# Performance work log

Hardware: AMD Instinct MI355X
Metric: run time of the kernel (lower is better)

## Reference

```python
import jax, jax.numpy as jnp
import numpy as np

NUM_FEATURE = 50


def setup_inputs() -> dict:
    key = jax.random.key(0)
    k1, = jax.random.split(key, 1)
    T = 500000
    query = jax.random.normal(k1, (T, NUM_FEATURE), dtype=jnp.float32)
    # Learned params exactly as the torch module initializes them:
    # ql.weight filled with 1 (shape [1, 50] -> we keep [50]), qW scalar 1.0
    ql_w = jnp.ones((NUM_FEATURE,), dtype=jnp.float32)
    qW = jnp.asarray(1.0, dtype=jnp.float32)
    return {"query": query, "ql_w": ql_w, "qW": qW}


def reference(query, ql_w, qW):
    # scores[i] = ql(tanh(qW * query[i]))  -> [T]
    scores = jnp.tanh(qW * query) @ ql_w
    # alpha = softmax(scores) over the T dimension (stable, single pass)
    alpha = jax.nn.softmax(scores, axis=0)
    # z = sum_i alpha[i] * query[i]  -> [NUM_FEATURE]
    z = alpha @ query
    return z
```

## Files before the change

kernel.cpp:

```cpp
#include <hip/hip_runtime.h>
#include <math.h>

#define NF 50
#define REC 52
#define NBLK 512
#define LOG2E 1.44269504f

#define DPP_QXOR1 0xB1
#define DPP_QXOR2 0x4E
#define DPP_ROR4  0x124
#define DPP_ROR8  0x128

__device__ __forceinline__ float dpp_add(float v, int ctrl) {
    float t;
    switch (ctrl) {
      case DPP_QXOR1: t = __int_as_float(__builtin_amdgcn_update_dpp(0, __float_as_int(v), DPP_QXOR1, 0xF, 0xF, true)); break;
      case DPP_QXOR2: t = __int_as_float(__builtin_amdgcn_update_dpp(0, __float_as_int(v), DPP_QXOR2, 0xF, 0xF, true)); break;
      case DPP_ROR4:  t = __int_as_float(__builtin_amdgcn_update_dpp(0, __float_as_int(v), DPP_ROR4,  0xF, 0xF, true)); break;
      default:        t = __int_as_float(__builtin_amdgcn_update_dpp(0, __float_as_int(v), DPP_ROR8,  0xF, 0xF, true)); break;
    }
    return v + t;
}

__global__ __launch_bounds__(512, 4) void attn_pass1(
    const float* __restrict__ query, const float* __restrict__ ql_w,
    const float* __restrict__ qWp, float* __restrict__ ws,
    int T, int totalGroups)
{
    const float qW = qWp[0];
    const int tid = threadIdx.x;
    const int q   = tid & 3;
    const int g   = blockIdx.x * 128 + (tid >> 2);

    float2 w01[7];
    #pragma unroll
    for (int t = 0; t < 6; ++t) {
        const int s = q + 4 * t;
        w01[t] = *(const float2*)(ql_w + 2 * s);
    }
    w01[6] = (q == 0) ? *(const float2*)(ql_w + 48) : make_float2(0.f, 0.f);
    const int d6 = (q == 0) ? 192 : 160;

    float sw = 0.f, saw = 0.f;
    #pragma unroll
    for (int t = 0; t < 7; ++t) {
        sw  += w01[t].x + w01[t].y;
        saw += fabsf(w01[t].x) + fabsf(w01[t].y);
    }
    sw  = dpp_add(dpp_add(sw,  DPP_QXOR1), DPP_QXOR2);
    saw = dpp_add(dpp_add(saw, DPP_QXOR1), DPP_QXOR2);
    const float M0  = (saw > 80.f) ? (saw - 80.f) : 0.f;
    const float c2  = 2.f * qW * LOG2E;
    const float K   = (sw - M0) * LOG2E;
    const float n2l = -2.f * LOG2E;

    float2 z[7];
    #pragma unroll
    for (int t = 0; t < 7; ++t) z[t] = make_float2(0.f, 0.f);
    float se = 0.f;

    const int G = totalGroups;
    const char* rp = (const char*)(query + (size_t)g * NF) + (q << 3);
    const size_t step = (size_t)G * NF * sizeof(float);

    for (int row = g; row < T; row += G, rp += step) {
        float2 x0 = *(const float2*)(rp);
        float2 x1 = *(const float2*)(rp + 32);
        float2 x2 = *(const float2*)(rp + 64);
        float2 x3 = *(const float2*)(rp + 96);
        float2 x4 = *(const float2*)(rp + 128);
        float2 x5 = *(const float2*)(rp + 160);
        float2 x6 = *(const float2*)(rp + d6);

        float p = 0.f;
        {
            float r;
            r = __builtin_amdgcn_rcpf(__builtin_amdgcn_exp2f(c2 * x0.x) + 1.f); p = fmaf(w01[0].x, r, p);
            r = __builtin_amdgcn_rcpf(__builtin_amdgcn_exp2f(c2 * x0.y) + 1.f); p = fmaf(w01[0].y, r, p);
            r = __builtin_amdgcn_rcpf(__builtin_amdgcn_exp2f(c2 * x1.x) + 1.f); p = fmaf(w01[1].x, r, p);
            r = __builtin_amdgcn_rcpf(__builtin_amdgcn_exp2f(c2 * x1.y) + 1.f); p = fmaf(w01[1].y, r, p);
            r = __builtin_amdgcn_rcpf(__builtin_amdgcn_exp2f(c2 * x2.x) + 1.f); p = fmaf(w01[2].x, r, p);
            r = __builtin_amdgcn_rcpf(__builtin_amdgcn_exp2f(c2 * x2.y) + 1.f); p = fmaf(w01[2].y, r, p);
            r = __builtin_amdgcn_rcpf(__builtin_amdgcn_exp2f(c2 * x3.x) + 1.f); p = fmaf(w01[3].x, r, p);
            r = __builtin_amdgcn_rcpf(__builtin_amdgcn_exp2f(c2 * x3.y) + 1.f); p = fmaf(w01[3].y, r, p);
            r = __builtin_amdgcn_rcpf(__builtin_amdgcn_exp2f(c2 * x4.x) + 1.f); p = fmaf(w01[4].x, r, p);
            r = __builtin_amdgcn_rcpf(__builtin_amdgcn_exp2f(c2 * x4.y) + 1.f); p = fmaf(w01[4].y, r, p);
            r = __builtin_amdgcn_rcpf(__builtin_amdgcn_exp2f(c2 * x5.x) + 1.f); p = fmaf(w01[5].x, r, p);
            r = __builtin_amdgcn_rcpf(__builtin_amdgcn_exp2f(c2 * x5.y) + 1.f); p = fmaf(w01[5].y, r, p);
            r = __builtin_amdgcn_rcpf(__builtin_amdgcn_exp2f(c2 * x6.x) + 1.f); p = fmaf(w01[6].x, r, p);
            r = __builtin_amdgcn_rcpf(__builtin_amdgcn_exp2f(c2 * x6.y) + 1.f); p = fmaf(w01[6].y, r, p);
        }
        p = dpp_add(dpp_add(p, DPP_QXOR1), DPP_QXOR2);
        const float e = __builtin_amdgcn_exp2f(fmaf(p, n2l, K));

        se += e;
        z[0].x = fmaf(e, x0.x, z[0].x); z[0].y = fmaf(e, x0.y, z[0].y);
        z[1].x = fmaf(e, x1.x, z[1].x); z[1].y = fmaf(e, x1.y, z[1].y);
        z[2].x = fmaf(e, x2.x, z[2].x); z[2].y = fmaf(e, x2.y, z[2].y);
        z[3].x = fmaf(e, x3.x, z[3].x); z[3].y = fmaf(e, x3.y, z[3].y);
        z[4].x = fmaf(e, x4.x, z[4].x); z[4].y = fmaf(e, x4.y, z[4].y);
        z[5].x = fmaf(e, x5.x, z[5].x); z[5].y = fmaf(e, x5.y, z[5].y);
        z[6].x = fmaf(e, x6.x, z[6].x); z[6].y = fmaf(e, x6.y, z[6].y);
    }

    #pragma unroll
    for (int t = 0; t < 7; ++t) {
        z[t].x = dpp_add(dpp_add(z[t].x, DPP_ROR4), DPP_ROR8);
        z[t].y = dpp_add(dpp_add(z[t].y, DPP_ROR4), DPP_ROR8);
    }
    se = dpp_add(dpp_add(se, DPP_ROR4), DPP_ROR8);

    __shared__ float sz[32][REC];
    if ((tid & 15) < 4) {
        const int eidx = tid >> 4;
        #pragma unroll
        for (int t = 0; t < 6; ++t) {
            const int s = q + 4 * t;
            *(float2*)&sz[eidx][2 * s] = z[t];
        }
        if (q == 0) {
            *(float2*)&sz[eidx][48] = z[6];
            sz[eidx][50] = se;
            sz[eidx][51] = 0.f;
        }
    }
    __syncthreads();

    if (tid < 51) {
        float acc = 0.f;
        #pragma unroll
        for (int h = 0; h < 32; ++h) acc += sz[h][tid];
        ws[(size_t)blockIdx.x * REC + tid] = acc;
    }
}

__global__ __launch_bounds__(1024) void attn_pass2(
    const float* __restrict__ ws, float* __restrict__ out, int B)
{
    __shared__ float zacc[16][REC];
    const int tid = threadIdx.x;
    const int w = tid >> 6, lane = tid & 63;

    if (lane < 51) {
        float acc = 0.f;
        int b = w;
        for (; b + 112 < B; b += 128) {
            acc += ws[(size_t)(b      ) * REC + lane]
                 + ws[(size_t)(b +  16) * REC + lane]
                 + ws[(size_t)(b +  32) * REC + lane]
                 + ws[(size_t)(b +  48) * REC + lane]
                 + ws[(size_t)(b +  64) * REC + lane]
                 + ws[(size_t)(b +  80) * REC + lane]
                 + ws[(size_t)(b +  96) * REC + lane]
                 + ws[(size_t)(b + 112) * REC + lane];
        }
        for (; b < B; b += 16)
            acc += ws[(size_t)b * REC + lane];
        zacc[w][lane] = acc;
    }
    __syncthreads();
    if (tid < NF) {
        float Z = 0.f, S = 0.f;
        #pragma unroll
        for (int h = 0; h < 16; ++h) { Z += zacc[h][tid]; S += zacc[h][50]; }
        out[tid] = Z / S;
    }
}

extern "C" void kernel_launch(void* const* d_in, const int* in_sizes, int n_in,
                              void* d_out, int out_size, void* d_ws, size_t ws_size,
                              hipStream_t stream) {
    const float* query = (const float*)d_in[0];
    const float* ql_w  = (const float*)d_in[1];
    const float* qW    = (const float*)d_in[2];
    float* out = (float*)d_out;
    float* ws  = (float*)d_ws;

    const int T = in_sizes[0] / NF;

    int B = NBLK;
    size_t need = (size_t)B * REC * sizeof(float);
    if (ws_size < need) {
        B = (int)(ws_size / (REC * sizeof(float)));
        if (B < 1) B = 1;
    }

    const int totalGroups = B * 128;
    hipLaunchKernelGGL(attn_pass1, dim3(B), dim3(512), 0, stream,
                       query, ql_w, qW, ws, T, totalGroups);
    hipLaunchKernelGGL(attn_pass2, dim3(1), dim3(1024), 0, stream,
                       ws, out, B);
}
```

Before: 25.71 us.

## Split each row across eight lanes instead of four and double block count

Result: slower. 27.88 us (+8.5%).

```diff
diff --git a/kernel.cpp b/kernel.cpp
--- a/kernel.cpp
+++ b/kernel.cpp
@@ -3,12 +3,12 @@
 
 #define NF 50
 #define REC 52
-#define NBLK 512
+#define NBLK 1024
 #define LOG2E 1.44269504f
 
 #define DPP_QXOR1 0xB1
 #define DPP_QXOR2 0x4E
-#define DPP_ROR4  0x124
+#define DPP_HMIRR 0x141
 #define DPP_ROR8  0x128
 
 __device__ __forceinline__ float dpp_add(float v, int ctrl) {
@@ -16,110 +16,86 @@
     switch (ctrl) {
       case DPP_QXOR1: t = __int_as_float(__builtin_amdgcn_update_dpp(0, __float_as_int(v), DPP_QXOR1, 0xF, 0xF, true)); break;
       case DPP_QXOR2: t = __int_as_float(__builtin_amdgcn_update_dpp(0, __float_as_int(v), DPP_QXOR2, 0xF, 0xF, true)); break;
-      case DPP_ROR4:  t = __int_as_float(__builtin_amdgcn_update_dpp(0, __float_as_int(v), DPP_ROR4,  0xF, 0xF, true)); break;
+      case DPP_HMIRR: t = __int_as_float(__builtin_amdgcn_update_dpp(0, __float_as_int(v), DPP_HMIRR, 0xF, 0xF, true)); break;
       default:        t = __int_as_float(__builtin_amdgcn_update_dpp(0, __float_as_int(v), DPP_ROR8,  0xF, 0xF, true)); break;
     }
     return v + t;
 }
 
-__global__ __launch_bounds__(512, 4) void attn_pass1(
+__global__ __launch_bounds__(512, 8) void attn_pass1(
     const float* __restrict__ query, const float* __restrict__ ql_w,
     const float* __restrict__ qWp, float* __restrict__ ws,
     int T, int totalGroups)
 {
     const float qW = qWp[0];
     const int tid = threadIdx.x;
-    const int q   = tid & 3;
-    const int g   = blockIdx.x * 128 + (tid >> 2);
+    const int l   = tid & 7;
+    const int g   = blockIdx.x * 64 + (tid >> 3);
 
-    float2 w01[7];
-    #pragma unroll
-    for (int t = 0; t < 6; ++t) {
-        const int s = q + 4 * t;
-        w01[t] = *(const float2*)(ql_w + 2 * s);
-    }
-    w01[6] = (q == 0) ? *(const float2*)(ql_w + 48) : make_float2(0.f, 0.f);
-    const int d6 = (q == 0) ? 192 : 160;
+    const float2 zf2 = make_float2(0.f, 0.f);
+    float2 w0 = *(const float2*)(ql_w + 2 * l);
+    float2 w1 = *(const float2*)(ql_w + 2 * (l + 8));
+    float2 w2 = *(const float2*)(ql_w + 2 * (l + 16));
+    float2 w3 = (l == 0) ? *(const float2*)(ql_w + 48) : zf2;
+    const int d3 = (l == 0) ? 192 : 128;
 
-    float sw = 0.f, saw = 0.f;
-    #pragma unroll
-    for (int t = 0; t < 7; ++t) {
-        sw  += w01[t].x + w01[t].y;
-        saw += fabsf(w01[t].x) + fabsf(w01[t].y);
-    }
-    sw  = dpp_add(dpp_add(sw,  DPP_QXOR1), DPP_QXOR2);
-    saw = dpp_add(dpp_add(saw, DPP_QXOR1), DPP_QXOR2);
+    float sw  = (w0.x + w0.y) + (w1.x + w1.y) + (w2.x + w2.y) + (w3.x + w3.y);
+    float saw = fabsf(w0.x) + fabsf(w0.y) + fabsf(w1.x) + fabsf(w1.y)
+              + fabsf(w2.x) + fabsf(w2.y) + fabsf(w3.x) + fabsf(w3.y);
+    sw  = dpp_add(dpp_add(dpp_add(sw,  DPP_QXOR1), DPP_QXOR2), DPP_HMIRR);
+    saw = dpp_add(dpp_add(dpp_add(saw, DPP_QXOR1), DPP_QXOR2), DPP_HMIRR);
     const float M0  = (saw > 80.f) ? (saw - 80.f) : 0.f;
     const float c2  = 2.f * qW * LOG2E;
     const float K   = (sw - M0) * LOG2E;
     const float n2l = -2.f * LOG2E;
 
-    float2 z[7];
-    #pragma unroll
-    for (int t = 0; t < 7; ++t) z[t] = make_float2(0.f, 0.f);
+    float2 z0 = zf2, z1 = zf2, z2 = zf2, z3 = zf2;
     float se = 0.f;
 
     const int G = totalGroups;
-    const char* rp = (const char*)(query + (size_t)g * NF) + (q << 3);
+    const char* rp = (const char*)(query + (size_t)g * NF) + (l << 3);
     const size_t step = (size_t)G * NF * sizeof(float);
 
     for (int row = g; row < T; row += G, rp += step) {
         float2 x0 = *(const float2*)(rp);
-        float2 x1 = *(const float2*)(rp + 32);
-        float2 x2 = *(const float2*)(rp + 64);
-        float2 x3 = *(const float2*)(rp + 96);
-        float2 x4 = *(const float2*)(rp + 128);
-        float2 x5 = *(const float2*)(rp + 160);
-        float2 x6 = *(const float2*)(rp + d6);
+        float2 x1 = *(const float2*)(rp + 64);
+        float2 x2 = *(const float2*)(rp + 128);
+        float2 x3 = *(const float2*)(rp + d3);
 
-        float p = 0.f;
-        {
-            float r;
-            r = __builtin_amdgcn_rcpf(__builtin_amdgcn_exp2f(c2 * x0.x) + 1.f); p = fmaf(w01[0].x, r, p);
-            r = __builtin_amdgcn_rcpf(__builtin_amdgcn_exp2f(c2 * x0.y) + 1.f); p = fmaf(w01[0].y, r, p);
-            r = __builtin_amdgcn_rcpf(__builtin_amdgcn_exp2f(c2 * x1.x) + 1.f); p = fmaf(w01[1].x, r, p);
-            r = __builtin_amdgcn_rcpf(__builtin_amdgcn_exp2f(c2 * x1.y) + 1.f); p = fmaf(w01[1].y, r, p);
-            r = __builtin_amdgcn_rcpf(__builtin_amdgcn_exp2f(c2 * x2.x) + 1.f); p = fmaf(w01[2].x, r, p);
-            r = __builtin_amdgcn_rcpf(__builtin_amdgcn_exp2f(c2 * x2.y) + 1.f); p = fmaf(w01[2].y, r, p);
-            r = __builtin_amdgcn_rcpf(__builtin_amdgcn_exp2f(c2 * x3.x) + 1.f); p = fmaf(w01[3].x, r, p);
-            r = __builtin_amdgcn_rcpf(__builtin_amdgcn_exp2f(c2 * x3.y) + 1.f); p = fmaf(w01[3].y, r, p);
-            r = __builtin_amdgcn_rcpf(__builtin_amdgcn_exp2f(c2 * x4.x) + 1.f); p = fmaf(w01[4].x, r, p);
-            r = __builtin_amdgcn_rcpf(__builtin_amdgcn_exp2f(c2 * x4.y) + 1.f); p = fmaf(w01[4].y, r, p);
-            r = __builtin_amdgcn_rcpf(__builtin_amdgcn_exp2f(c2 * x5.x) + 1.f); p = fmaf(w01[5].x, r, p);
-            r = __builtin_amdgcn_rcpf(__builtin_amdgcn_exp2f(c2 * x5.y) + 1.f); p = fmaf(w01[5].y, r, p);
-            r = __builtin_amdgcn_rcpf(__builtin_amdgcn_exp2f(c2 * x6.x) + 1.f); p = fmaf(w01[6].x, r, p);
-            r = __builtin_amdgcn_rcpf(__builtin_amdgcn_exp2f(c2 * x6.y) + 1.f); p = fmaf(w01[6].y, r, p);
-        }
-        p = dpp_add(dpp_add(p, DPP_QXOR1), DPP_QXOR2);
+        float p = 0.f, r;
+        r = __builtin_amdgcn_rcpf(__builtin_amdgcn_exp2f(c2 * x0.x) + 1.f); p = fmaf(w0.x, r, p);
+        r = __builtin_amdgcn_rcpf(__builtin_amdgcn_exp2f(c2 * x0.y) + 1.f); p = fmaf(w0.y, r, p);
+        r = __builtin_amdgcn_rcpf(__builtin_amdgcn_exp2f(c2 * x1.x) + 1.f); p = fmaf(w1.x, r, p);
+        r = __builtin_amdgcn_rcpf(__builtin_amdgcn_exp2f(c2 * x1.y) + 1.f); p = fmaf(w1.y, r, p);
+        r = __builtin_amdgcn_rcpf(__builtin_amdgcn_exp2f(c2 * x2.x) + 1.f); p = fmaf(w2.x, r, p);
+        r = __builtin_amdgcn_rcpf(__builtin_amdgcn_exp2f(c2 * x2.y) + 1.f); p = fmaf(w2.y, r, p);
+        r = __builtin_amdgcn_rcpf(__builtin_amdgcn_exp2f(c2 * x3.x) + 1.f); p = fmaf(w3.x, r, p);
+        r = __builtin_amdgcn_rcpf(__builtin_amdgcn_exp2f(c2 * x3.y) + 1.f); p = fmaf(w3.y, r, p);
+
+        p = dpp_add(dpp_add(dpp_add(p, DPP_QXOR1), DPP_QXOR2), DPP_HMIRR);
         const float e = __builtin_amdgcn_exp2f(fmaf(p, n2l, K));
 
         se += e;
-        z[0].x = fmaf(e, x0.x, z[0].x); z[0].y = fmaf(e, x0.y, z[0].y);
-        z[1].x = fmaf(e, x1.x, z[1].x); z[1].y = fmaf(e, x1.y, z[1].y);
-        z[2].x = fmaf(e, x2.x, z[2].x); z[2].y = fmaf(e, x2.y, z[2].y);
-        z[3].x = fmaf(e, x3.x, z[3].x); z[3].y = fmaf(e, x3.y, z[3].y);
-        z[4].x = fmaf(e, x4.x, z[4].x); z[4].y = fmaf(e, x4.y, z[4].y);
-        z[5].x = fmaf(e, x5.x, z[5].x); z[5].y = fmaf(e, x5.y, z[5].y);
-        z[6].x = fmaf(e, x6.x, z[6].x); z[6].y = fmaf(e, x6.y, z[6].y);
+        z0.x = fmaf(e, x0.x, z0.x); z0.y = fmaf(e, x0.y, z0.y);
+        z1.x = fmaf(e, x1.x, z1.x); z1.y = fmaf(e, x1.y, z1.y);
+        z2.x = fmaf(e, x2.x, z2.x); z2.y = fmaf(e, x2.y, z2.y);
+        z3.x = fmaf(e, x3.x, z3.x); z3.y = fmaf(e, x3.y, z3.y);
     }
 
-    #pragma unroll
-    for (int t = 0; t < 7; ++t) {
-        z[t].x = dpp_add(dpp_add(z[t].x, DPP_ROR4), DPP_ROR8);
-        z[t].y = dpp_add(dpp_add(z[t].y, DPP_ROR4), DPP_ROR8);
-    }
-    se = dpp_add(dpp_add(se, DPP_ROR4), DPP_ROR8);
+    z0.x = dpp_add(z0.x, DPP_ROR8); z0.y = dpp_add(z0.y, DPP_ROR8);
+    z1.x = dpp_add(z1.x, DPP_ROR8); z1.y = dpp_add(z1.y, DPP_ROR8);
+    z2.x = dpp_add(z2.x, DPP_ROR8); z2.y = dpp_add(z2.y, DPP_ROR8);
+    z3.x = dpp_add(z3.x, DPP_ROR8); z3.y = dpp_add(z3.y, DPP_ROR8);
+    se   = dpp_add(se,   DPP_ROR8);
 
     __shared__ float sz[32][REC];
-    if ((tid & 15) < 4) {
+    if ((tid & 15) < 8) {
         const int eidx = tid >> 4;
-        #pragma unroll
-        for (int t = 0; t < 6; ++t) {
-            const int s = q + 4 * t;
-            *(float2*)&sz[eidx][2 * s] = z[t];
-        }
-        if (q == 0) {
-            *(float2*)&sz[eidx][48] = z[6];
+        *(float2*)&sz[eidx][2 * l]        = z0;
+        *(float2*)&sz[eidx][2 * (l + 8)]  = z1;
+        *(float2*)&sz[eidx][2 * (l + 16)] = z2;
+        if (l == 0) {
+            *(float2*)&sz[eidx][48] = z3;
             sz[eidx][50] = se;
             sz[eidx][51] = 0.f;
         }
@@ -185,7 +161,7 @@
         if (B < 1) B = 1;
     }
 
-    const int totalGroups = B * 128;
+    const int totalGroups = B * 64;
     hipLaunchKernelGGL(attn_pass1, dim3(B), dim3(512), 0, stream,
                        query, ql_w, qW, ws, T, totalGroups);
     hipLaunchKernelGGL(attn_pass2, dim3(1), dim3(1024), 0, stream,
```

## Fuse two-pass reduction into one cooperative kernel with grid sync

Applied to the files above, without the earlier changes.

Result: slower. 92.12 us (+258.3%).

```diff
diff --git a/kernel.cpp b/kernel.cpp
--- a/kernel.cpp
+++ b/kernel.cpp
@@ -1,4 +1,5 @@
 #include <hip/hip_runtime.h>
+#include <hip/hip_cooperative_groups.h>
 #include <math.h>
 
 #define NF 50
@@ -22,10 +23,10 @@
     return v + t;
 }
 
-__global__ __launch_bounds__(512, 4) void attn_pass1(
+__global__ __launch_bounds__(512, 4) void attn_fused(
     const float* __restrict__ query, const float* __restrict__ ql_w,
     const float* __restrict__ qWp, float* __restrict__ ws,
-    int T, int totalGroups)
+    float* __restrict__ out, int T, int totalGroups, int nBlocks)
 {
     const float qW = qWp[0];
     const int tid = threadIdx.x;
@@ -132,38 +133,31 @@
         for (int h = 0; h < 32; ++h) acc += sz[h][tid];
         ws[(size_t)blockIdx.x * REC + tid] = acc;
     }
-}
 
-__global__ __launch_bounds__(1024) void attn_pass2(
-    const float* __restrict__ ws, float* __restrict__ out, int B)
-{
-    __shared__ float zacc[16][REC];
-    const int tid = threadIdx.x;
-    const int w = tid >> 6, lane = tid & 63;
+    cooperative_groups::this_grid().sync();
 
-    if (lane < 51) {
-        float acc = 0.f;
-        int b = w;
-        for (; b + 112 < B; b += 128) {
-            acc += ws[(size_t)(b      ) * REC + lane]
-                 + ws[(size_t)(b +  16) * REC + lane]
-                 + ws[(size_t)(b +  32) * REC + lane]
-                 + ws[(size_t)(b +  48) * REC + lane]
-                 + ws[(size_t)(b +  64) * REC + lane]
-                 + ws[(size_t)(b +  80) * REC + lane]
-                 + ws[(size_t)(b +  96) * REC + lane]
-                 + ws[(size_t)(b + 112) * REC + lane];
+    if (blockIdx.x == 0) {
+        const int w = tid >> 6, lane = tid & 63;
+        if (lane < 51) {
+            float acc = 0.f;
+            int b = w;
+            for (; b + 24 < nBlocks; b += 32) {
+                acc += ws[(size_t)(b     ) * REC + lane]
+                     + ws[(size_t)(b +  8) * REC + lane]
+                     + ws[(size_t)(b + 16) * REC + lane]
+                     + ws[(size_t)(b + 24) * REC + lane];
+            }
+            for (; b < nBlocks; b += 8)
+                acc += ws[(size_t)b * REC + lane];
+            sz[w][lane] = acc;
         }
-        for (; b < B; b += 16)
-            acc += ws[(size_t)b * REC + lane];
-        zacc[w][lane] = acc;
-    }
-    __syncthreads();
-    if (tid < NF) {
-        float Z = 0.f, S = 0.f;
-        #pragma unroll
-        for (int h = 0; h < 16; ++h) { Z += zacc[h][tid]; S += zacc[h][50]; }
-        out[tid] = Z / S;
+        __syncthreads();
+        if (tid < NF) {
+            float Z = 0.f, S = 0.f;
+            #pragma unroll
+            for (int h = 0; h < 8; ++h) { Z += sz[h][tid]; S += sz[h][50]; }
+            out[tid] = Z / S;
+        }
     }
 }
 
@@ -176,7 +170,7 @@
     float* out = (float*)d_out;
     float* ws  = (float*)d_ws;
 
-    const int T = in_sizes[0] / NF;
+    int T = in_sizes[0] / NF;
 
     int B = NBLK;
     size_t need = (size_t)B * REC * sizeof(float);
@@ -185,9 +179,9 @@
         if (B < 1) B = 1;
     }
 
-    const int totalGroups = B * 128;
-    hipLaunchKernelGGL(attn_pass1, dim3(B), dim3(512), 0, stream,
-                       query, ql_w, qW, ws, T, totalGroups);
-    hipLaunchKernelGGL(attn_pass2, dim3(1), dim3(1024), 0, stream,
-                       ws, out, B);
+    int totalGroups = B * 128;
+    void* args[] = { (void*)&query, (void*)&ql_w, (void*)&qW, (void*)&ws,
+                     (void*)&out, (void*)&T, (void*)&totalGroups, (void*)&B };
+    hipLaunchCooperativeKernel((void*)attn_fused, dim3(B), dim3(512),
+                               args, 0, stream);
 }
```

## Process row pairs with float4 loads in a new even-T pass1 kernel

Applied to the files above, without the earlier changes.

Result: slower. 26.51 us (+3.1%).

```diff
diff --git a/kernel.cpp b/kernel.cpp
--- a/kernel.cpp
+++ b/kernel.cpp
@@ -22,7 +22,9 @@
     return v + t;
 }
 
-__global__ __launch_bounds__(512, 4) void attn_pass1(
+#define RCPE(v) __builtin_amdgcn_rcpf(__builtin_amdgcn_exp2f(c2 * (v)) + 1.f)
+
+__global__ __launch_bounds__(512, 4) void attn_pass1_even(
     const float* __restrict__ query, const float* __restrict__ ql_w,
     const float* __restrict__ qWp, float* __restrict__ ws,
     int T, int totalGroups)
@@ -32,6 +34,156 @@
     const int q   = tid & 3;
     const int g   = blockIdx.x * 128 + (tid >> 2);
 
+    float4 w4[6];
+    #pragma unroll
+    for (int t = 0; t < 6; ++t) {
+        const int c = q + 4 * t;
+        const int f0 = 4*c, f1 = 4*c+1, f2 = 4*c+2, f3 = 4*c+3;
+        w4[t] = make_float4(ql_w[f0 >= 50 ? f0-50 : f0],
+                            ql_w[f1 >= 50 ? f1-50 : f1],
+                            ql_w[f2 >= 50 ? f2-50 : f2],
+                            ql_w[f3 >= 50 ? f3-50 : f3]);
+    }
+    const float wsc = ql_w[46 + q];
+
+    float sw = wsc, saw = fabsf(wsc);
+    #pragma unroll
+    for (int t = 0; t < 6; ++t) {
+        sw  += (w4[t].x + w4[t].y) + (w4[t].z + w4[t].w);
+        saw += (fabsf(w4[t].x) + fabsf(w4[t].y)) + (fabsf(w4[t].z) + fabsf(w4[t].w));
+    }
+    sw  = dpp_add(dpp_add(sw,  DPP_QXOR1), DPP_QXOR2) * 0.5f;
+    saw = dpp_add(dpp_add(saw, DPP_QXOR1), DPP_QXOR2) * 0.5f;
+    const float M0  = (saw > 80.f) ? (saw - 80.f) : 0.f;
+    const float c2  = 2.f * qW * LOG2E;
+    const float K   = (sw - M0) * LOG2E;
+    const float n2l = -2.f * LOG2E;
+
+    float4 w3r0, w3r1;
+    if (q == 0) { w3r0 = make_float4(w4[3].x, w4[3].y, 0.f, 0.f);
+                  w3r1 = make_float4(0.f, 0.f, w4[3].z, w4[3].w); }
+    else        { w3r0 = make_float4(0.f, 0.f, 0.f, 0.f);
+                  w3r1 = w4[3]; }
+    const float m3 = (q == 0) ? 1.f : 0.f;
+
+    float4 z0 = {0,0,0,0}, z1 = {0,0,0,0}, z2 = {0,0,0,0},
+           z3 = {0,0,0,0}, z4 = {0,0,0,0}, z5 = {0,0,0,0};
+    float zsc = 0.f, se = 0.f;
+
+    const int TP = T >> 1;
+    const int G  = totalGroups;
+    const char* rp = (const char*)query + (size_t)g * 400 + (q << 4);
+    const int off_s = 384 - 12 * q;
+    const size_t step = (size_t)G * 400;
+
+    for (int pr = g; pr < TP; pr += G, rp += step) {
+        float4 x0 = *(const float4*)(rp);
+        float4 x1 = *(const float4*)(rp + 64);
+        float4 x2 = *(const float4*)(rp + 128);
+        float4 x3 = *(const float4*)(rp + 192);
+        float4 x4 = *(const float4*)(rp + 256);
+        float4 x5 = *(const float4*)(rp + 320);
+        float  xs = *(const float*)(rp + off_s);
+
+        float p0 = 0.f, p1 = 0.f, r;
+        r = RCPE(x0.x); p0 = fmaf(w4[0].x, r, p0);
+        r = RCPE(x0.y); p0 = fmaf(w4[0].y, r, p0);
+        r = RCPE(x0.z); p0 = fmaf(w4[0].z, r, p0);
+        r = RCPE(x0.w); p0 = fmaf(w4[0].w, r, p0);
+        r = RCPE(x1.x); p0 = fmaf(w4[1].x, r, p0);
+        r = RCPE(x1.y); p0 = fmaf(w4[1].y, r, p0);
+        r = RCPE(x1.z); p0 = fmaf(w4[1].z, r, p0);
+        r = RCPE(x1.w); p0 = fmaf(w4[1].w, r, p0);
+        r = RCPE(x2.x); p0 = fmaf(w4[2].x, r, p0);
+        r = RCPE(x2.y); p0 = fmaf(w4[2].y, r, p0);
+        r = RCPE(x2.z); p0 = fmaf(w4[2].z, r, p0);
+        r = RCPE(x2.w); p0 = fmaf(w4[2].w, r, p0);
+        {
+            float r3x = RCPE(x3.x), r3y = RCPE(x3.y);
+            float r3z = RCPE(x3.z), r3w = RCPE(x3.w);
+            p0 = fmaf(w3r0.x, r3x, p0); p0 = fmaf(w3r0.y, r3y, p0);
+            p1 = fmaf(w3r1.x, r3x, p1); p1 = fmaf(w3r1.y, r3y, p1);
+            p1 = fmaf(w3r1.z, r3z, p1); p1 = fmaf(w3r1.w, r3w, p1);
+        }
+        r = RCPE(x4.x); p1 = fmaf(w4[4].x, r, p1);
+        r = RCPE(x4.y); p1 = fmaf(w4[4].y, r, p1);
+        r = RCPE(x4.z); p1 = fmaf(w4[4].z, r, p1);
+        r = RCPE(x4.w); p1 = fmaf(w4[4].w, r, p1);
+        r = RCPE(x5.x); p1 = fmaf(w4[5].x, r, p1);
+        r = RCPE(x5.y); p1 = fmaf(w4[5].y, r, p1);
+        r = RCPE(x5.z); p1 = fmaf(w4[5].z, r, p1);
+        r = RCPE(x5.w); p1 = fmaf(w4[5].w, r, p1);
+        r = RCPE(xs);   p1 = fmaf(wsc,     r, p1);
+
+        p0 = dpp_add(dpp_add(p0, DPP_QXOR1), DPP_QXOR2);
+        p1 = dpp_add(dpp_add(p1, DPP_QXOR1), DPP_QXOR2);
+        const float e0 = __builtin_amdgcn_exp2f(fmaf(p0, n2l, K));
+        const float e1 = __builtin_amdgcn_exp2f(fmaf(p1, n2l, K));
+        se += e0 + e1;
+        const float ez3 = fmaf(m3, e0 - e1, e1);
+
+        z0.x = fmaf(e0, x0.x, z0.x); z0.y = fmaf(e0, x0.y, z0.y);
+        z0.z = fmaf(e0, x0.z, z0.z); z0.w = fmaf(e0, x0.w, z0.w);
+        z1.x = fmaf(e0, x1.x, z1.x); z1.y = fmaf(e0, x1.y, z1.y);
+        z1.z = fmaf(e0, x1.z, z1.z); z1.w = fmaf(e0, x1.w, z1.w);
+        z2.x = fmaf(e0, x2.x, z2.x); z2.y = fmaf(e0, x2.y, z2.y);
+        z2.z = fmaf(e0, x2.z, z2.z); z2.w = fmaf(e0, x2.w, z2.w);
+        z3.x = fmaf(ez3, x3.x, z3.x); z3.y = fmaf(ez3, x3.y, z3.y);
+        z3.z = fmaf(e1,  x3.z, z3.z); z3.w = fmaf(e1,  x3.w, z3.w);
+        z4.x = fmaf(e1, x4.x, z4.x); z4.y = fmaf(e1, x4.y, z4.y);
+        z4.z = fmaf(e1, x4.z, z4.z); z4.w = fmaf(e1, x4.w, z4.w);
+        z5.x = fmaf(e1, x5.x, z5.x); z5.y = fmaf(e1, x5.y, z5.y);
+        z5.z = fmaf(e1, x5.z, z5.z); z5.w = fmaf(e1, x5.w, z5.w);
+        zsc  = fmaf(e1, xs, zsc);
+    }
+
+    #define RED(v) v = dpp_add(dpp_add(v, DPP_ROR4), DPP_ROR8)
+    RED(z0.x); RED(z0.y); RED(z0.z); RED(z0.w);
+    RED(z1.x); RED(z1.y); RED(z1.z); RED(z1.w);
+    RED(z2.x); RED(z2.y); RED(z2.z); RED(z2.w);
+    RED(z3.x); RED(z3.y); RED(z3.z); RED(z3.w);
+    RED(z4.x); RED(z4.y); RED(z4.z); RED(z4.w);
+    RED(z5.x); RED(z5.y); RED(z5.z); RED(z5.w);
+    RED(zsc);  RED(se);
+    #undef RED
+
+    __shared__ float s100[32][104];
+    const int eidx = tid >> 4;
+    if ((tid & 15) < 4) {
+        *(float4*)&s100[eidx][4 * (q     )] = z0;
+        *(float4*)&s100[eidx][4 * (q +  4)] = z1;
+        *(float4*)&s100[eidx][4 * (q +  8)] = z2;
+        *(float4*)&s100[eidx][4 * (q + 12)] = z3;
+        *(float4*)&s100[eidx][4 * (q + 16)] = z4;
+        *(float4*)&s100[eidx][4 * (q + 20)] = z5;
+        s100[eidx][96 + q] = zsc;
+        if (q == 0) s100[eidx][100] = se;
+    }
+    __syncthreads();
+
+    if (tid < 50) {
+        float acc = 0.f;
+        #pragma unroll
+        for (int h = 0; h < 32; ++h) acc += s100[h][tid] + s100[h][tid + 50];
+        ws[(size_t)blockIdx.x * REC + tid] = acc;
+    } else if (tid == 50) {
+        float acc = 0.f;
+        #pragma unroll
+        for (int h = 0; h < 32; ++h) acc += s100[h][100];
+        ws[(size_t)blockIdx.x * REC + 50] = acc;
+    }
+}
+
+__global__ __launch_bounds__(512, 4) void attn_pass1_f2(
+    const float* __restrict__ query, const float* __restrict__ ql_w,
+    const float* __restrict__ qWp, float* __restrict__ ws,
+    int T, int totalGroups)
+{
+    const float qW = qWp[0];
+    const int tid = threadIdx.x;
+    const int q   = tid & 3;
+    const int g   = blockIdx.x * 128 + (tid >> 2);
+
     float2 w01[7];
     #pragma unroll
     for (int t = 0; t < 6; ++t) {
@@ -72,24 +224,22 @@
         float2 x5 = *(const float2*)(rp + 160);
         float2 x6 = *(const float2*)(rp + d6);
 
-        float p = 0.f;
-        {
-            float r;
-            r = __builtin_amdgcn_rcpf(__builtin_amdgcn_exp2f(c2 * x0.x) + 1.f); p = fmaf(w01[0].x, r, p);
-            r = __builtin_amdgcn_rcpf(__builtin_amdgcn_exp2f(c2 * x0.y) + 1.f); p = fmaf(w01[0].y, r, p);
-            r = __builtin_amdgcn_rcpf(__builtin_amdgcn_exp2f(c2 * x1.x) + 1.f); p = fmaf(w01[1].x, r, p);
-            r = __builtin_amdgcn_rcpf(__builtin_amdgcn_exp2f(c2 * x1.y) + 1.f); p = fmaf(w01[1].y, r, p);
-            r = __builtin_amdgcn_rcpf(__builtin_amdgcn_exp2f(c2 * x2.x) + 1.f); p = fmaf(w01[2].x, r, p);
-            r = __builtin_amdgcn_rcpf(__builtin_amdgcn_exp2f(c2 * x2.y) + 1.f); p = fmaf(w01[2].y, r, p);
-            r = __builtin_amdgcn_rcpf(__builtin_amdgcn_exp2f(c2 * x3.x) + 1.f); p = fmaf(w01[3].x, r, p);
-            r = __builtin_amdgcn_rcpf(__builtin_amdgcn_exp2f(c2 * x3.y) + 1.f); p = fmaf(w01[3].y, r, p);
-            r = __builtin_amdgcn_rcpf(__builtin_amdgcn_exp2f(c2 * x4.x) + 1.f); p = fmaf(w01[4].x, r, p);
-            r = __builtin_amdgcn_rcpf(__builtin_amdgcn_exp2f(c2 * x4.y) + 1.f); p = fmaf(w01[4].y, r, p);
-            r = __builtin_amdgcn_rcpf(__builtin_amdgcn_exp2f(c2 * x5.x) + 1.f); p = fmaf(w01[5].x, r, p);
-            r = __builtin_amdgcn_rcpf(__builtin_amdgcn_exp2f(c2 * x5.y) + 1.f); p = fmaf(w01[5].y, r, p);
-            r = __builtin_amdgcn_rcpf(__builtin_amdgcn_exp2f(c2 * x6.x) + 1.f); p = fmaf(w01[6].x, r, p);
-            r = __builtin_amdgcn_rcpf(__builtin_amdgcn_exp2f(c2 * x6.y) + 1.f); p = fmaf(w01[6].y, r, p);
-        }
+        float p = 0.f, r;
+        r = RCPE(x0.x); p = fmaf(w01[0].x, r, p);
+        r = RCPE(x0.y); p = fmaf(w01[0].y, r, p);
+        r = RCPE(x1.x); p = fmaf(w01[1].x, r, p);
+        r = RCPE(x1.y); p = fmaf(w01[1].y, r, p);
+        r = RCPE(x2.x); p = fmaf(w01[2].x, r, p);
+        r = RCPE(x2.y); p = fmaf(w01[2].y, r, p);
+        r = RCPE(x3.x); p = fmaf(w01[3].x, r, p);
+        r = RCPE(x3.y); p = fmaf(w01[3].y, r, p);
+        r = RCPE(x4.x); p = fmaf(w01[4].x, r, p);
+        r = RCPE(x4.y); p = fmaf(w01[4].y, r, p);
+        r = RCPE(x5.x); p = fmaf(w01[5].x, r, p);
+        r = RCPE(x5.y); p = fmaf(w01[5].y, r, p);
+        r = RCPE(x6.x); p = fmaf(w01[6].x, r, p);
+        r = RCPE(x6.y); p = fmaf(w01[6].y, r, p);
+
         p = dpp_add(dpp_add(p, DPP_QXOR1), DPP_QXOR2);
         const float e = __builtin_amdgcn_exp2f(fmaf(p, n2l, K));
 
@@ -186,8 +336,13 @@
     }
 
     const int totalGroups = B * 128;
-    hipLaunchKernelGGL(attn_pass1, dim3(B), dim3(512), 0, stream,
-                       query, ql_w, qW, ws, T, totalGroups);
+    if ((T & 1) == 0) {
+        hipLaunchKernelGGL(attn_pass1_even, dim3(B), dim3(512), 0, stream,
+                           query, ql_w, qW, ws, T, totalGroups);
+    } else {
+        hipLaunchKernelGGL(attn_pass1_f2, dim3(B), dim3(512), 0, stream,
+                           query, ql_w, qW, ws, T, totalGroups);
+    }
     hipLaunchKernelGGL(attn_pass2, dim3(1), dim3(1024), 0, stream,
                        ws, out, B);
 }
```
